# Performance work log

Hardware: AMD Instinct MI355X
Metric: run time of the kernel (lower is better)

## Reference

```python
import jax, jax.numpy as jnp
import numpy as np

N = 100000   # nodes
E = 1600000  # edges
NF = 128     # nfeat
NH = 64      # nhid
NC = 16      # nclass
C = 1.0      # curvature
EPS = 1e-15
PROJ_EPS = 4e-3  # float32 boundary eps used by HGCN PoincareBall
SQC = C ** 0.5


def _norm(v):
    return jnp.maximum(jnp.linalg.norm(v, axis=-1, keepdims=True), EPS)


def _artanh(v):
    return jnp.arctanh(jnp.clip(v, -1.0 + 1e-7, 1.0 - 1e-7))


def proj(p):
    # clip to the open ball of radius (1-eps)/sqrt(c)
    n = _norm(p)
    maxnorm = (1.0 - PROJ_EPS) / SQC
    return jnp.where(n > maxnorm, p / n * maxnorm, p)


def expmap0(u):
    n = _norm(u)
    return jnp.tanh(SQC * n) * u / (SQC * n)


def logmap0(p):
    n = _norm(p)
    return _artanh(SQC * n) * p / (SQC * n)


def mobius_add(x, y):
    x2 = jnp.sum(x * x, axis=-1, keepdims=True)
    y2 = jnp.sum(y * y, axis=-1, keepdims=True)
    xy = jnp.sum(x * y, axis=-1, keepdims=True)
    num = (1.0 + 2.0 * C * xy + C * y2) * x + (1.0 - C * x2) * y
    den = 1.0 + 2.0 * C * xy + (C ** 2) * x2 * y2
    return num / jnp.maximum(den, EPS)


def mobius_matvec(W, p):
    # W: [out, in], p: [N, in] on the ball
    pn = _norm(p)
    mp = p @ W.T  # [N, out]
    mpn = jnp.linalg.norm(mp, axis=-1, keepdims=True)
    res = jnp.tanh(mpn / pn * _artanh(SQC * pn)) * mp / (SQC * jnp.maximum(mpn, EPS))
    return jnp.where(mpn <= EPS, jnp.zeros_like(res), res)


def setup_inputs() -> dict:
    key = jax.random.key(0)
    ks = jax.random.split(key, 16)
    inp = {
        "x": jax.random.normal(ks[0], (N, NF), dtype=jnp.float32),
        "src": jax.random.randint(ks[1], (E,), 0, N, dtype=jnp.int32),
        "dst": jax.random.randint(ks[2], (E,), 0, N, dtype=jnp.int32),
        "adj_val": jax.random.uniform(ks[3], (E,), dtype=jnp.float32) * 0.0625,
        "W1": jax.random.normal(ks[4], (NH, NF), dtype=jnp.float32) / np.sqrt(NF),
        "b1": jnp.zeros((NH,), dtype=jnp.float32),
        "W2": jax.random.normal(ks[5], (NH, NH), dtype=jnp.float32) / np.sqrt(NH),
        "b2": jnp.zeros((NH,), dtype=jnp.float32),
        "W3": jax.random.normal(ks[6], (NH, NH), dtype=jnp.float32) / np.sqrt(NH),
        "b3": jnp.zeros((NH,), dtype=jnp.float32),
        "W4": jax.random.normal(ks[7], (NH // 2, NH), dtype=jnp.float32) / np.sqrt(NH),
        "b4": jnp.zeros((NH // 2,), dtype=jnp.float32),
        "W5": jax.random.normal(ks[8], (NC, NH // 2), dtype=jnp.float32) / np.sqrt(NH // 2),
        "b5": jnp.zeros((NC,), dtype=jnp.float32),
    }
    return inp


def _hgc_layer(h, W, b, src, dst, adj_val):
    # HypLinear: mobius matvec + hyperbolic bias
    res = proj(mobius_matvec(W, h))
    hyp_b = proj(expmap0(b[None, :]))
    res = proj(mobius_add(res, hyp_b))
    # HypAgg: aggregate in tangent space at origin via sparse adj
    ht = logmap0(res)                                   # [N, d]
    msg = adj_val[:, None] * ht[src]                    # [E, d]
    agg = jax.ops.segment_sum(msg, dst, num_segments=N)  # [N, d]
    res = proj(expmap0(agg))
    # HypAct: relu in tangent space, re-map to ball
    res = proj(expmap0(jax.nn.relu(logmap0(res))))
    return res


def reference(x, src, dst, adj_val, W1, b1, W2, b2, W3, b3, W4, b4, W5, b5):
    h = proj(expmap0(x))  # map Euclidean features to the ball (proj_tan0 = identity)
    h = _hgc_layer(h, W1, b1, src, dst, adj_val)
    h = _hgc_layer(h, W2, b2, src, dst, adj_val)
    h = _hgc_layer(h, W3, b3, src, dst, adj_val)
    t = logmap0(h)  # back to tangent space for the Euclidean head
    z = jax.nn.relu(t @ W4.T + b4)
    return jax.nn.log_softmax(z @ W5.T + b5, axis=-1)  # [N, nclass]
```

## Files before the change

### kernel.cpp

```cpp
#include <hip/hip_runtime.h>
#include <hip/hip_bf16.h>
#include <hip/hip_fp16.h>
#include <math.h>

#define NFEAT 128
#define NHID  64
#define ATH996 3.106303f
#define CHUNK 4096

typedef __attribute__((ext_vector_type(8))) short short8;
typedef __attribute__((ext_vector_type(4))) float floatx4;
typedef unsigned short ushort_t;
typedef unsigned long long u64;

__device__ __forceinline__ float wave_sum(float v) {
#pragma unroll
    for (int m = 1; m < 64; m <<= 1) v += __shfl_xor(v, m, 64);
    return v;
}

__device__ __forceinline__ float fast_tanh(float x) {
    float e = __expf(2.f * x);
    return 1.f - 2.f / (e + 1.f);
}

__device__ __forceinline__ float artanh_clip(float v) {
    const float lim = 0.99999988f;
    v = fminf(fmaxf(v, -lim), lim);
    return 0.5f * __logf((1.f + v) / (1.f - v));
}

__device__ __forceinline__ unsigned pack2(float a, float b) {
    __hip_bfloat16 x = __float2bfloat16(a), y = __float2bfloat16(b);
    ushort_t ux = *(ushort_t*)&x, uy = *(ushort_t*)&y;
    return (unsigned)ux | ((unsigned)uy << 16);
}

__device__ __forceinline__ ushort_t f2bf(float f) {
    __hip_bfloat16 h = __float2bfloat16(f);
    return *(ushort_t*)&h;
}

__device__ __forceinline__ float pe_adj(unsigned p) {
    return __half2float(__ushort_as_half((ushort_t)(p & 0x7fffu)));
}


__global__ __launch_bounds__(256) void k_bscan(const int* __restrict__ gBktCnt,
        int* __restrict__ gBktBase, int* __restrict__ gCur,
        int* __restrict__ off, int nb, int n, int e) {
    __shared__ int s[256];
    int tid = threadIdx.x;
    int base = tid * 4;
    int c0 = (base + 0 < nb) ? gBktCnt[base + 0] : 0;
    int c1 = (base + 1 < nb) ? gBktCnt[base + 1] : 0;
    int c2 = (base + 2 < nb) ? gBktCnt[base + 2] : 0;
    int c3 = (base + 3 < nb) ? gBktCnt[base + 3] : 0;
    int tsum = c0 + c1 + c2 + c3;
    s[tid] = tsum; __syncthreads();
    for (int o = 1; o < 256; o <<= 1) {
        int v = (tid >= o) ? s[tid - o] : 0;
        __syncthreads();
        s[tid] += v;
        __syncthreads();
    }
    int ex = s[tid] - tsum;
    int e0 = ex, e1 = ex + c0, e2 = ex + c0 + c1, e3 = ex + c0 + c1 + c2;
    if (base + 0 < nb) { gBktBase[base + 0] = e0; gCur[base + 0] = e0; }
    if (base + 1 < nb) { gBktBase[base + 1] = e1; gCur[base + 1] = e1; }
    if (base + 2 < nb) { gBktBase[base + 2] = e2; gCur[base + 2] = e2; }
    if (base + 3 < nb) { gBktBase[base + 3] = e3; gCur[base + 3] = e3; }
    if (tid == 255) gBktBase[nb] = s[255];
    if (tid == 0) off[n] = e;
}

__global__ __launch_bounds__(256) void k_bscatter(const int* __restrict__ dst,
        const int* __restrict__ src, const float* __restrict__ adj,
        int* __restrict__ gCur, u64* __restrict__ gStage, int e, int nb) {
    __shared__ u64 stage[CHUNK];
    __shared__ int cnt[512], excl[512], rcnt[512], myBase[512], s[256];
    int tid = threadIdx.x;
    int start = blockIdx.x * CHUNK, end = min(e, start + CHUNK);
    for (int t = tid; t < nb; t += 256) { cnt[t] = 0; rcnt[t] = 0; }
    __syncthreads();
    for (int i = start + tid; i < end; i += 256)
        atomicAdd(&cnt[dst[i] >> 8], 1);
    __syncthreads();
    int v0 = (2 * tid < nb) ? cnt[2 * tid] : 0;
    int v1 = (2 * tid + 1 < nb) ? cnt[2 * tid + 1] : 0;
    int tsum = v0 + v1;
    s[tid] = tsum; __syncthreads();
    for (int o = 1; o < 256; o <<= 1) {
        int v = (tid >= o) ? s[tid - o] : 0;
        __syncthreads();
        s[tid] += v;
        __syncthreads();
    }
    int ex = s[tid] - tsum;
    if (2 * tid < nb) excl[2 * tid] = ex;
    if (2 * tid + 1 < nb) excl[2 * tid + 1] = ex + v0;
    __syncthreads();
    for (int t = tid; t < nb; t += 256)
        if (cnt[t]) myBase[t] = atomicAdd(&gCur[t], cnt[t]);
    for (int i = start + tid; i < end; i += 256) {
        int d = dst[i];
        int b = d >> 8;
        unsigned ab = (unsigned)__half_as_ushort(__float2half(adj[i])) & 0x7fffu;
        u64 u = ((u64)(unsigned)d << 32) |
                (u64)(((unsigned)src[i] << 15) | ab);
        int r = atomicAdd(&rcnt[b], 1);
        stage[excl[b] + r] = u;
    }
    __syncthreads();
    int sz = end - start;
    for (int j = tid; j < sz; j += 256) {
        u64 u = stage[j];
        int b = (int)(u >> 40) & 0x1ff;
        gStage[myBase[b] + (j - excl[b])] = u;
    }
}

__global__ __launch_bounds__(256) void k_bfinal(const u64* __restrict__ gStage,
        const int* __restrict__ gBktBase, int* __restrict__ off,
        unsigned* __restrict__ pe, int n) {
    __shared__ int ncnt[256], nexcl[256], rcnt[256], s[256];
    int tid = threadIdx.x, b = blockIdx.x;
    int ebeg = gBktBase[b], eend = gBktBase[b + 1];
    int nbeg = b << 8;
    ncnt[tid] = 0; rcnt[tid] = 0;
    __syncthreads();
    for (int j = ebeg + tid; j < eend; j += 256) {
        int dl = ((int)(gStage[j] >> 32) & 0x1ffff) - nbeg;
        atomicAdd(&ncnt[dl], 1);
    }
    __syncthreads();
    int v = ncnt[tid];
    s[tid] = v; __syncthreads();
    for (int o = 1; o < 256; o <<= 1) {
        int t2 = (tid >= o) ? s[tid - o] : 0;
        __syncthreads();
        s[tid] += t2;
        __syncthreads();
    }
    nexcl[tid] = s[tid] - v;
    if (nbeg + tid < n) off[nbeg + tid] = ebeg + nexcl[tid];
    __syncthreads();
    for (int j = ebeg + tid; j < eend; j += 256) {
        u64 u = gStage[j];
        int dl = ((int)(u >> 32) & 0x1ffff) - nbeg;
        int r = atomicAdd(&rcnt[dl], 1);
        pe[ebeg + nexcl[dl] + r] = (unsigned)u;
    }
}

__global__ __launch_bounds__(256) void k_prep(
        const float* __restrict__ W1, const float* __restrict__ W2,
        const float* __restrict__ W3, const float* __restrict__ W4,
        const float* __restrict__ W5, const float* __restrict__ b1,
        const float* __restrict__ b2, const float* __restrict__ b3,
        ushort_t* __restrict__ Bpk1, ushort_t* __restrict__ Bpk2,
        ushort_t* __restrict__ Bpk3, ushort_t* __restrict__ Bpk4,
        ushort_t* __restrict__ Bpk5, float* __restrict__ hbs,
        float* __restrict__ hbns, int* __restrict__ gBktCnt, int nb) {
    int bid = blockIdx.x, tid = threadIdx.x;
    if (bid >= 75) {
        for (int t = tid; t < nb; t += 256) gBktCnt[t] = 0;
        return;
    }
    if (bid < 64) {
        const float* W; ushort_t* Bpk; int K, o;
        if (bid < 32)      { W = W1; Bpk = Bpk1; K = 128; o = bid * 256 + tid; }
        else if (bid < 48) { W = W2; Bpk = Bpk2; K = 64;  o = (bid - 32) * 256 + tid; }
        else               { W = W3; Bpk = Bpk3; K = 64;  o = (bid - 48) * 256 + tid; }
        int j = o & 7, c = (o >> 3) & 15, nf = (o >> 7) & 3, hi = (o >> 9) & 3,
            ks = o >> 11;
        Bpk[o] = f2bf(W[(nf * 16 + c) * K + ks * 32 + hi * 8 + j]);
    } else if (bid < 72) {
        int o = (bid - 64) * 256 + tid;
        int j = o & 7, c = (o >> 3) & 15, nf = (o >> 7) & 1, hi = (o >> 8) & 3,
            ks = o >> 10;
        Bpk4[o] = f2bf(W4[(nf * 16 + c) * 64 + ks * 32 + hi * 8 + j]);
    } else if (bid < 74) {
        int o = (bid - 72) * 256 + tid;
        if (o < 512) {
            int j = o & 7, c = (o >> 3) & 15, hi = o >> 7;
            Bpk5[o] = f2bf(W5[c * 32 + hi * 8 + j]);
        }
    } else {
        if (tid < 192) {
            int wv = tid >> 6, lane = tid & 63;
            const float* b = (wv == 0) ? b1 : (wv == 1) ? b2 : b3;
            float bv = b[lane];
            float bn = fmaxf(sqrtf(wave_sum(bv * bv)), 1e-15f);
            float th = fast_tanh(bn);
            float f = th / bn;
            float hn = th;
            if (th > 0.996f) { f = 0.996f / bn; hn = 0.996f; }
            hbs[wv * 64 + lane] = bv * f;
            if (lane == 0) hbns[wv] = hn;
        }
    }
}

__device__ __forceinline__ void epi_vals(const float vin[4], float pn,
        float hbn, const float* __restrict__ hb, int c, float outv[4]) {
    float pp = 0.f;
#pragma unroll
    for (int nf = 0; nf < 4; ++nf) pp += vin[nf] * vin[nf];
#pragma unroll
    for (int m = 1; m < 16; m <<= 1) pp += __shfl_xor(pp, m, 64);
    float mpn = sqrtf(pp);
    float an = artanh_clip(pn);
    if (hbn <= 1e-15f) {
        float targ = (mpn / pn) * an;
        float scale = (targ > ATH996) ? (ATH996 / mpn) : (an / pn);
        if (mpn <= 1e-15f) scale = 0.f;
#pragma unroll
        for (int nf = 0; nf < 4; ++nf) outv[nf] = vin[nf] * scale;
    } else {
        float targ = (mpn / pn) * an;
        float th = fast_tanh(targ);
        float rn = fminf(th, 0.996f);
        float rs = (mpn <= 1e-15f) ? 0.f : (rn / mpn);
        float res[4], xyp = 0.f;
#pragma unroll
        for (int nf = 0; nf < 4; ++nf) {
            res[nf] = vin[nf] * rs;
            xyp += res[nf] * hb[nf * 16 + c];
        }
#pragma unroll
        for (int m = 1; m < 16; m <<= 1) xyp += __shfl_xor(xyp, m, 64);
        float x2 = rn * rn, y2 = hbn * hbn;
        float den = fmaxf(1.f + 2.f * xyp + x2 * y2, 1e-15f);
        float ca = (1.f + 2.f * xyp + y2) / den, cb = (1.f - x2) / den;
        float mv[4], mm = 0.f;
#pragma unroll
        for (int nf = 0; nf < 4; ++nf) {
            mv[nf] = ca * res[nf] + cb * hb[nf * 16 + c];
            mm += mv[nf] * mv[nf];
        }
#pragma unroll
        for (int m = 1; m < 16; m <<= 1) mm += __shfl_xor(mm, m, 64);
        float mn = sqrtf(mm);
        float mc = fminf(fmaxf(mn, 1e-15f), 0.996f);
        float msc = ((mn > 0.996f) ? (0.996f / mn) : 1.f) * artanh_clip(mc) / mc;
#pragma unroll
        for (int nf = 0; nf < 4; ++nf) outv[nf] = mv[nf] * msc;
    }
}

__global__ __launch_bounds__(256) void k_gemm1_hist(
        const float* __restrict__ x, const ushort_t* __restrict__ Bpk,
        const float* __restrict__ hb, const float* __restrict__ hbn_p,
        ushort_t* __restrict__ htout, int n, int gBlocks,
        const int* __restrict__ dst, int* __restrict__ gBktCnt, int e, int nb) {
    constexpr int RB = 256;
    __shared__ __align__(16) unsigned char As[64 * RB];
    __shared__ float pns[64], fs[64];
    __shared__ int cnt[512];
    int tid = threadIdx.x;
    if ((int)blockIdx.x >= gBlocks) {
        for (int t = tid; t < nb; t += 256) cnt[t] = 0;
        __syncthreads();
        int start = ((int)blockIdx.x - gBlocks) * CHUNK, end = min(e, start + CHUNK);
        for (int i = start + tid; i < end; i += 256)
            atomicAdd(&cnt[dst[i] >> 8], 1);
        __syncthreads();
        for (int t = tid; t < nb; t += 256)
            if (cnt[t]) atomicAdd(&gBktCnt[t], cnt[t]);
        return;
    }
    int wv = tid >> 6, lane = tid & 63;
    int grp = lane >> 4, l = lane & 15;
    int rowBase = blockIdx.x * 64;
#pragma unroll
    for (int it = 0; it < 4; ++it) {
        int row = wv * 16 + it * 4 + grp, rg = rowBase + row;
        float4 va = make_float4(0.f, 0.f, 0.f, 0.f), vb = va;
        if (rg < n) {
            const float4* xr = (const float4*)(x + (size_t)rg * NFEAT + l * 8);
            va = xr[0]; vb = xr[1];
        }
        uint4 pk;
        pk.x = pack2(va.x, va.y); pk.y = pack2(va.z, va.w);
        pk.z = pack2(vb.x, vb.y); pk.w = pack2(vb.z, vb.w);
        unsigned byte = (unsigned)(row * RB + l * 16) ^ ((row & 7) << 4);
        *(uint4*)(As + byte) = pk;
        float ss = va.x * va.x + va.y * va.y + va.z * va.z + va.w * va.w +
                   vb.x * vb.x + vb.y * vb.y + vb.z * vb.z + vb.w * vb.w;
#pragma unroll
        for (int m = 1; m < 16; m <<= 1) ss += __shfl_xor(ss, m, 64);
        if (l == 0) {
            float nr = fmaxf(sqrtf(ss), 1e-15f);
            float th = fast_tanh(nr);
            float f = th / nr;
            float pn = fmaxf(th, 1e-15f);
            if (th > 0.996f) { f = 0.996f / nr; pn = 0.996f; }
            pns[row] = pn; fs[row] = f;
        }
    }
    int hi = lane >> 4, c = lane & 15;
    short8 bf[4][4];
#pragma unroll
    for (int ks = 0; ks < 4; ++ks)
#pragma unroll
        for (int nf = 0; nf < 4; ++nf)
            bf[ks][nf] = *(const short8*)(Bpk + (((size_t)(ks * 4 + hi) * 4 + nf) * 16 + c) * 8);
    floatx4 acc[4];
#pragma unroll
    for (int nf = 0; nf < 4; ++nf)
#pragma unroll
        for (int r = 0; r < 4; ++r) acc[nf][r] = 0.f;
    int arow = wv * 16 + c;
#pragma unroll
    for (int ks = 0; ks < 4; ++ks) {
        unsigned byte = (unsigned)(arow * RB + ks * 64 + hi * 16) ^ ((arow & 7) << 4);
        short8 af = *(const short8*)(As + byte);
#pragma unroll
        for (int nf = 0; nf < 4; ++nf)
            acc[nf] = __builtin_amdgcn_mfma_f32_16x16x32_bf16(af, bf[ks][nf], acc[nf], 0, 0, 0);
    }
    float hbn = hbn_p[0];
#pragma unroll
    for (int r = 0; r < 4; ++r) {
        int row = wv * 16 + hi * 4 + r, rg = rowBase + row;
        float f = fs[row];
        float vin[4], outv[4];
#pragma unroll
        for (int nf = 0; nf < 4; ++nf) vin[nf] = acc[nf][r] * f;
        epi_vals(vin, pns[row], hbn, hb, c, outv);
        if (rg < n) {
#pragma unroll
            for (int nf = 0; nf < 4; ++nf)
                htout[(size_t)rg * 64 + nf * 16 + c] = f2bf(outv[nf]);
        }
    }
}

__global__ __launch_bounds__(256) void k_gemm64(
        const ushort_t* __restrict__ h, const float* __restrict__ nrm_in,
        const ushort_t* __restrict__ Bpk, const float* __restrict__ hb,
        const float* __restrict__ hbn_p, ushort_t* __restrict__ htout, int n) {
    constexpr int RB = 128;
    __shared__ __align__(16) unsigned char As[64 * RB];
    int tid = threadIdx.x, wv = tid >> 6, lane = tid & 63;
    int grp = lane >> 4, l = lane & 15;
    int rowBase = blockIdx.x * 64;
#pragma unroll
    for (int it = 0; it < 4; ++it) {
        int row = wv * 16 + it * 4 + grp, rg = rowBase + row;
        uint2 pk = make_uint2(0u, 0u);
        if (rg < n) pk = *(const uint2*)(h + (size_t)rg * 64 + l * 4);
        unsigned byte = (unsigned)(row * RB + l * 8) ^ ((row & 7) << 4);
        *(uint2*)(As + byte) = pk;
    }
    int hi = lane >> 4, c = lane & 15;
    short8 bf[2][4];
#pragma unroll
    for (int ks = 0; ks < 2; ++ks)
#pragma unroll
        for (int nf = 0; nf < 4; ++nf)
            bf[ks][nf] = *(const short8*)(Bpk + (((size_t)(ks * 4 + hi) * 4 + nf) * 16 + c) * 8);
    floatx4 acc[4];
#pragma unroll
    for (int nf = 0; nf < 4; ++nf)
#pragma unroll
        for (int r = 0; r < 4; ++r) acc[nf][r] = 0.f;
    int arow = wv * 16 + c;
#pragma unroll
    for (int ks = 0; ks < 2; ++ks) {
        unsigned byte = (unsigned)(arow * RB + ks * 64 + hi * 16) ^ ((arow & 7) << 4);
        short8 af = *(const short8*)(As + byte);
#pragma unroll
        for (int nf = 0; nf < 4; ++nf)
            acc[nf] = __builtin_amdgcn_mfma_f32_16x16x32_bf16(af, bf[ks][nf], acc[nf], 0, 0, 0);
    }
    float hbn = hbn_p[0];
#pragma unroll
    for (int r = 0; r < 4; ++r) {
        int row = wv * 16 + hi * 4 + r, rg = rowBase + row;
        float pn = (rg < n) ? nrm_in[rg] : 1e-15f;
        float vin[4], outv[4];
#pragma unroll
        for (int nf = 0; nf < 4; ++nf) vin[nf] = acc[nf][r];
        epi_vals(vin, pn, hbn, hb, c, outv);
        if (rg < n) {
#pragma unroll
            for (int nf = 0; nf < 4; ++nf)
                htout[(size_t)rg * 64 + nf * 16 + c] = f2bf(outv[nf]);
        }
    }
}

template <bool TANGENT_OUT>
__global__ __launch_bounds__(256) void k_agg_act(
        const ushort_t* __restrict__ ht, const int* __restrict__ off,
        const unsigned* __restrict__ pe, ushort_t* __restrict__ hout,
        float* __restrict__ nrm_out, int n) {
    int tid = threadIdx.x;
    int grp = tid >> 4, l = tid & 15;
    int gw = (tid & 63) >> 4;
    int node = blockIdx.x * 16 + grp;
    if (node >= n) return;
    int beg = off[node], end = off[node + 1];
    const char* hb8 = (const char*)ht + l * 8;
    float ac[4][4] = {};
    for (int e = beg; e < end; e += 16) {
        int cnt = end - e;
        unsigned pv = (l < cnt) ? pe[e + l] : 0u;
        uint2 rr[16];
#pragma unroll
        for (int u = 0; u < 16; ++u) {
            unsigned p = __shfl(pv, (gw << 4) | u, 64);
            unsigned row = (u < cnt) ? (p >> 15) : 0u;
            rr[u] = *(const uint2*)(hb8 + ((size_t)row << 7));
        }
#pragma unroll
        for (int u = 0; u < 16; ++u) {
            unsigned p = __shfl(pv, (gw << 4) | u, 64);
            float w = (u < cnt) ? pe_adj(p) : 0.f;
            ac[u & 3][0] = fmaf(w, __uint_as_float(rr[u].x << 16), ac[u & 3][0]);
            ac[u & 3][1] = fmaf(w, __uint_as_float(rr[u].x & 0xffff0000u), ac[u & 3][1]);
            ac[u & 3][2] = fmaf(w, __uint_as_float(rr[u].y << 16), ac[u & 3][2]);
            ac[u & 3][3] = fmaf(w, __uint_as_float(rr[u].y & 0xffff0000u), ac[u & 3][3]);
        }
    }
    float f0 = (ac[0][0] + ac[1][0]) + (ac[2][0] + ac[3][0]);
    float f1 = (ac[0][1] + ac[1][1]) + (ac[2][1] + ac[3][1]);
    float f2 = (ac[0][2] + ac[1][2]) + (ac[2][2] + ac[3][2]);
    float f3 = (ac[0][3] + ac[1][3]) + (ac[2][3] + ac[3][3]);
    float ss = f0 * f0 + f1 * f1 + f2 * f2 + f3 * f3;
#pragma unroll
    for (int m = 1; m < 16; m <<= 1) ss += __shfl_xor(ss, m, 64);
    float un = fmaxf(sqrtf(ss), 1e-15f);
    float thu = fast_tanh(un);
    float pf = thu / un, pn = thu;
    if (thu > 0.996f) { pf = 0.996f / un; pn = 0.996f; }
    float pnc = fmaxf(pn, 1e-15f);
    float ls = artanh_clip(pnc) / pnc * pf;
    float t0 = fmaxf(ls * f0, 0.f), t1 = fmaxf(ls * f1, 0.f);
    float t2 = fmaxf(ls * f2, 0.f), t3 = fmaxf(ls * f3, 0.f);
    float ss2 = t0 * t0 + t1 * t1 + t2 * t2 + t3 * t3;
#pragma unroll
    for (int m = 1; m < 16; m <<= 1) ss2 += __shfl_xor(ss2, m, 64);
    float tn = fmaxf(sqrtf(ss2), 1e-15f);
    uint2 ov;
    if (TANGENT_OUT) {
        float sc = (tn > ATH996) ? (ATH996 / tn) : 1.f;
        ov = make_uint2(pack2(t0 * sc, t1 * sc), pack2(t2 * sc, t3 * sc));
    } else {
        float tht = fast_tanh(tn);
        float rf = tht / tn, rn = tht;
        if (tht > 0.996f) { rf = 0.996f / tn; rn = 0.996f; }
        ov = make_uint2(pack2(rf * t0, rf * t1), pack2(rf * t2, rf * t3));
        if (l == 0) nrm_out[node] = fmaxf(rn, 1e-15f);
    }
    *(uint2*)((char*)hout + (size_t)node * 128 + l * 8) = ov;
}

__global__ __launch_bounds__(256) void k_head(
        const ushort_t* __restrict__ t_in, const ushort_t* __restrict__ Bpk4,
        const float* __restrict__ b4, const ushort_t* __restrict__ Bpk5,
        const float* __restrict__ b5, float* __restrict__ out, int n) {
    constexpr int RB = 128;
    __shared__ __align__(16) unsigned char As[64 * RB];
    __shared__ __align__(16) unsigned char Zs[4][16 * 80];
    int tid = threadIdx.x, wv = tid >> 6, lane = tid & 63;
    int grp = lane >> 4, l = lane & 15;
    int rowBase = blockIdx.x * 64;
#pragma unroll
    for (int it = 0; it < 4; ++it) {
        int row = wv * 16 + it * 4 + grp, rg = rowBase + row;
        uint2 pk = make_uint2(0u, 0u);
        if (rg < n) pk = *(const uint2*)(t_in + (size_t)rg * 64 + l * 4);
        unsigned byte = (unsigned)(row * RB + l * 8) ^ ((row & 7) << 4);
        *(uint2*)(As + byte) = pk;
    }
    int hi = lane >> 4, c = lane & 15;
    short8 bf4[2][2];
#pragma unroll
    for (int ks = 0; ks < 2; ++ks)
#pragma unroll
        for (int nf = 0; nf < 2; ++nf)
            bf4[ks][nf] = *(const short8*)(Bpk4 + (((size_t)(ks * 4 + hi) * 2 + nf) * 16 + c) * 8);
    floatx4 acc[2];
#pragma unroll
    for (int nf = 0; nf < 2; ++nf)
#pragma unroll
        for (int r = 0; r < 4; ++r) acc[nf][r] = 0.f;
    int arow = wv * 16 + c;
#pragma unroll
    for (int ks = 0; ks < 2; ++ks) {
        unsigned byte = (unsigned)(arow * RB + ks * 64 + hi * 16) ^ ((arow & 7) << 4);
        short8 af = *(const short8*)(As + byte);
#pragma unroll
        for (int nf = 0; nf < 2; ++nf)
            acc[nf] = __builtin_amdgcn_mfma_f32_16x16x32_bf16(af, bf4[ks][nf], acc[nf], 0, 0, 0);
    }
    float bb0 = b4[c], bb1 = b4[16 + c];
#pragma unroll
    for (int r = 0; r < 4; ++r) {
        int zr = hi * 4 + r;
        *(ushort_t*)(Zs[wv] + zr * 80 + c * 2) = f2bf(fmaxf(acc[0][r] + bb0, 0.f));
        *(ushort_t*)(Zs[wv] + zr * 80 + (16 + c) * 2) = f2bf(fmaxf(acc[1][r] + bb1, 0.f));
    }
    short8 bf5 = *(const short8*)(Bpk5 + ((size_t)(hi * 16 + c)) * 8);
    short8 zf = *(const short8*)(Zs[wv] + c * 80 + hi * 16);
    floatx4 acc5;
#pragma unroll
    for (int r = 0; r < 4; ++r) acc5[r] = 0.f;
    acc5 = __builtin_amdgcn_mfma_f32_16x16x32_bf16(zf, bf5, acc5, 0, 0, 0);
    float b5v = b5[c];
#pragma unroll
    for (int r = 0; r < 4; ++r) {
        float y = acc5[r] + b5v;
        float mx = y;
#pragma unroll
        for (int mk = 1; mk < 16; mk <<= 1) mx = fmaxf(mx, __shfl_xor(mx, mk, 64));
        float sm = __expf(y - mx);
#pragma unroll
        for (int mk = 1; mk < 16; mk <<= 1) sm += __shfl_xor(sm, mk, 64);
        int rg = rowBase + wv * 16 + hi * 4 + r;
        if (rg < n) out[(size_t)rg * 16 + c] = y - mx - __logf(sm);
    }
}

extern "C" void kernel_launch(void* const* d_in, const int* in_sizes, int n_in,
                              void* d_out, int out_size, void* d_ws, size_t ws_size,
                              hipStream_t stream) {
    const float* x   = (const float*)d_in[0];
    const int*   src = (const int*)d_in[1];
    const int*   dst = (const int*)d_in[2];
    const float* adj = (const float*)d_in[3];
    const float* W1  = (const float*)d_in[4];  const float* b1 = (const float*)d_in[5];
    const float* W2  = (const float*)d_in[6];  const float* b2 = (const float*)d_in[7];
    const float* W3  = (const float*)d_in[8];  const float* b3 = (const float*)d_in[9];
    const float* W4  = (const float*)d_in[10]; const float* b4 = (const float*)d_in[11];
    const float* W5  = (const float*)d_in[12]; const float* b5 = (const float*)d_in[13];
    float* out = (float*)d_out;

    const int N = in_sizes[0] / NFEAT;
    const int E = in_sizes[1];
    const int NB = (N + 255) >> 8;

    char* w = (char*)d_ws;
    auto alloc = [&](size_t bytes) {
        char* p = w; w += (bytes + 255) & ~(size_t)255; return p;
    };
    int* off      = (int*)alloc((size_t)(N + 1) * 4);
    int* gBktCnt  = (int*)alloc((size_t)NB * 4);
    int* gBktBase = (int*)alloc((size_t)(NB + 1) * 4);
    int* gCur     = (int*)alloc((size_t)NB * 4);
    u64* gStage   = (u64*)alloc((size_t)E * 8);
    unsigned* pe  = (unsigned*)alloc((size_t)E * 4);
    ushort_t* B   = (ushort_t*)alloc((size_t)N * 64 * 2);
    ushort_t* D   = (ushort_t*)alloc((size_t)N * 64 * 2);
    float* nrm    = (float*)alloc((size_t)N * 4);
    float* hbs    = (float*)alloc(192 * 4);
    float* hbns   = (float*)alloc(4 * 4);
    ushort_t* Bpk1 = (ushort_t*)alloc(8192 * 2);
    ushort_t* Bpk2 = (ushort_t*)alloc(4096 * 2);
    ushort_t* Bpk3 = (ushort_t*)alloc(4096 * 2);
    ushort_t* Bpk4 = (ushort_t*)alloc(2048 * 2);
    ushort_t* Bpk5 = (ushort_t*)alloc(512 * 2);

    dim3 blk(256);
    int aggBlocks  = (N + 15) / 16;
    int gemmBlocks = (N + 63) / 64;
    int sortBlocks = (E + CHUNK - 1) / CHUNK;

    k_prep<<<76, blk, 0, stream>>>(W1, W2, W3, W4, W5, b1, b2, b3,
                                   Bpk1, Bpk2, Bpk3, Bpk4, Bpk5, hbs, hbns,
                                   gBktCnt, NB);

    k_gemm1_hist<<<gemmBlocks + sortBlocks, blk, 0, stream>>>(
        x, Bpk1, hbs, hbns, B, N, gemmBlocks, dst, gBktCnt, E, NB);

    k_bscan<<<1, blk, 0, stream>>>(gBktCnt, gBktBase, gCur, off, NB, N, E);
    k_bscatter<<<sortBlocks, blk, 0, stream>>>(dst, src, adj, gCur, gStage, E, NB);
    k_bfinal<<<NB, blk, 0, stream>>>(gStage, gBktBase, off, pe, N);

    k_agg_act<false><<<aggBlocks, blk, 0, stream>>>(B, off, pe, D, nrm, N);
    k_gemm64<<<gemmBlocks, blk, 0, stream>>>(D, nrm, Bpk2, hbs + 64, hbns + 1, B, N);
    k_agg_act<false><<<aggBlocks, blk, 0, stream>>>(B, off, pe, D, nrm, N);
    k_gemm64<<<gemmBlocks, blk, 0, stream>>>(D, nrm, Bpk3, hbs + 128, hbns + 2, B, N);
    k_agg_act<true><<<aggBlocks, blk, 0, stream>>>(B, off, pe, D, nullptr, N);

    k_head<<<gemmBlocks, blk, 0, stream>>>(D, Bpk4, b4, Bpk5, b5, out, N);
}
```

Before: 222.5 us.

## Switch intermediate storage and MFMA to fp16 with packed half2 aggregation

```diff
diff --git a/kernel.cpp b/kernel.cpp
--- a/kernel.cpp
+++ b/kernel.cpp
@@ -1,5 +1,4 @@
 #include <hip/hip_runtime.h>
-#include <hip/hip_bf16.h>
 #include <hip/hip_fp16.h>
 #include <math.h>
 
@@ -8,7 +7,7 @@
 #define ATH996 3.106303f
 #define CHUNK 4096
 
-typedef __attribute__((ext_vector_type(8))) short short8;
+typedef __attribute__((ext_vector_type(8))) _Float16 half8;
 typedef __attribute__((ext_vector_type(4))) float floatx4;
 typedef unsigned short ushort_t;
 typedef unsigned long long u64;
@@ -30,19 +29,17 @@
     return 0.5f * __logf((1.f + v) / (1.f - v));
 }
 
-__device__ __forceinline__ unsigned pack2(float a, float b) {
-    __hip_bfloat16 x = __float2bfloat16(a), y = __float2bfloat16(b);
-    ushort_t ux = *(ushort_t*)&x, uy = *(ushort_t*)&y;
-    return (unsigned)ux | ((unsigned)uy << 16);
-}
-
-__device__ __forceinline__ ushort_t f2bf(float f) {
-    __hip_bfloat16 h = __float2bfloat16(f);
+__device__ __forceinline__ ushort_t f2h(float f) {
+    __half h = __float2half(f);
     return *(ushort_t*)&h;
 }
 
-__device__ __forceinline__ float pe_adj(unsigned p) {
-    return __half2float(__ushort_as_half((ushort_t)(p & 0x7fffu)));
+__device__ __forceinline__ unsigned pk2h(float a, float b) {
+    return (unsigned)f2h(a) | ((unsigned)f2h(b) << 16);
+}
+
+__device__ __forceinline__ __half pe_adjh(unsigned p) {
+    return __ushort_as_half((ushort_t)(p & 0x7fffu));
 }
 
 
@@ -174,17 +171,17 @@
         else               { W = W3; Bpk = Bpk3; K = 64;  o = (bid - 48) * 256 + tid; }
         int j = o & 7, c = (o >> 3) & 15, nf = (o >> 7) & 3, hi = (o >> 9) & 3,
             ks = o >> 11;
-        Bpk[o] = f2bf(W[(nf * 16 + c) * K + ks * 32 + hi * 8 + j]);
+        Bpk[o] = f2h(W[(nf * 16 + c) * K + ks * 32 + hi * 8 + j]);
     } else if (bid < 72) {
         int o = (bid - 64) * 256 + tid;
         int j = o & 7, c = (o >> 3) & 15, nf = (o >> 7) & 1, hi = (o >> 8) & 3,
             ks = o >> 10;
-        Bpk4[o] = f2bf(W4[(nf * 16 + c) * 64 + ks * 32 + hi * 8 + j]);
+        Bpk4[o] = f2h(W4[(nf * 16 + c) * 64 + ks * 32 + hi * 8 + j]);
     } else if (bid < 74) {
         int o = (bid - 72) * 256 + tid;
         if (o < 512) {
             int j = o & 7, c = (o >> 3) & 15, hi = o >> 7;
-            Bpk5[o] = f2bf(W5[c * 32 + hi * 8 + j]);
+            Bpk5[o] = f2h(W5[c * 32 + hi * 8 + j]);
         }
     } else {
         if (tid < 192) {
@@ -282,8 +279,8 @@
             va = xr[0]; vb = xr[1];
         }
         uint4 pk;
-        pk.x = pack2(va.x, va.y); pk.y = pack2(va.z, va.w);
-        pk.z = pack2(vb.x, vb.y); pk.w = pack2(vb.z, vb.w);
+        pk.x = pk2h(va.x, va.y); pk.y = pk2h(va.z, va.w);
+        pk.z = pk2h(vb.x, vb.y); pk.w = pk2h(vb.z, vb.w);
         unsigned byte = (unsigned)(row * RB + l * 16) ^ ((row & 7) << 4);
         *(uint4*)(As + byte) = pk;
         float ss = va.x * va.x + va.y * va.y + va.z * va.z + va.w * va.w +
@@ -300,12 +297,12 @@
         }
     }
     int hi = lane >> 4, c = lane & 15;
-    short8 bf[4][4];
+    half8 bf[4][4];
 #pragma unroll
     for (int ks = 0; ks < 4; ++ks)
 #pragma unroll
         for (int nf = 0; nf < 4; ++nf)
-            bf[ks][nf] = *(const short8*)(Bpk + (((size_t)(ks * 4 + hi) * 4 + nf) * 16 + c) * 8);
+            bf[ks][nf] = *(const half8*)(Bpk + (((size_t)(ks * 4 + hi) * 4 + nf) * 16 + c) * 8);
     floatx4 acc[4];
 #pragma unroll
     for (int nf = 0; nf < 4; ++nf)
@@ -315,10 +312,10 @@
 #pragma unroll
     for (int ks = 0; ks < 4; ++ks) {
         unsigned byte = (unsigned)(arow * RB + ks * 64 + hi * 16) ^ ((arow & 7) << 4);
-        short8 af = *(const short8*)(As + byte);
+        half8 af = *(const half8*)(As + byte);
 #pragma unroll
         for (int nf = 0; nf < 4; ++nf)
-            acc[nf] = __builtin_amdgcn_mfma_f32_16x16x32_bf16(af, bf[ks][nf], acc[nf], 0, 0, 0);
+            acc[nf] = __builtin_amdgcn_mfma_f32_16x16x32_f16(af, bf[ks][nf], acc[nf], 0, 0, 0);
     }
     float hbn = hbn_p[0];
 #pragma unroll
@@ -332,7 +329,7 @@
         if (rg < n) {
 #pragma unroll
             for (int nf = 0; nf < 4; ++nf)
-                htout[(size_t)rg * 64 + nf * 16 + c] = f2bf(outv[nf]);
+                htout[(size_t)rg * 64 + nf * 16 + c] = f2h(outv[nf]);
         }
     }
 }
@@ -355,12 +352,12 @@
         *(uint2*)(As + byte) = pk;
     }
     int hi = lane >> 4, c = lane & 15;
-    short8 bf[2][4];
+    half8 bf[2][4];
 #pragma unroll
     for (int ks = 0; ks < 2; ++ks)
 #pragma unroll
         for (int nf = 0; nf < 4; ++nf)
-            bf[ks][nf] = *(const short8*)(Bpk + (((size_t)(ks * 4 + hi) * 4 + nf) * 16 + c) * 8);
+            bf[ks][nf] = *(const half8*)(Bpk + (((size_t)(ks * 4 + hi) * 4 + nf) * 16 + c) * 8);
     floatx4 acc[4];
 #pragma unroll
     for (int nf = 0; nf < 4; ++nf)
@@ -370,10 +367,10 @@
 #pragma unroll
     for (int ks = 0; ks < 2; ++ks) {
         unsigned byte = (unsigned)(arow * RB + ks * 64 + hi * 16) ^ ((arow & 7) << 4);
-        short8 af = *(const short8*)(As + byte);
+        half8 af = *(const half8*)(As + byte);
 #pragma unroll
         for (int nf = 0; nf < 4; ++nf)
-            acc[nf] = __builtin_amdgcn_mfma_f32_16x16x32_bf16(af, bf[ks][nf], acc[nf], 0, 0, 0);
+            acc[nf] = __builtin_amdgcn_mfma_f32_16x16x32_f16(af, bf[ks][nf], acc[nf], 0, 0, 0);
     }
     float hbn = hbn_p[0];
 #pragma unroll
@@ -387,7 +384,7 @@
         if (rg < n) {
 #pragma unroll
             for (int nf = 0; nf < 4; ++nf)
-                htout[(size_t)rg * 64 + nf * 16 + c] = f2bf(outv[nf]);
+                htout[(size_t)rg * 64 + nf * 16 + c] = f2h(outv[nf]);
         }
     }
 }
@@ -399,36 +396,46 @@
         float* __restrict__ nrm_out, int n) {
     int tid = threadIdx.x;
     int grp = tid >> 4, l = tid & 15;
-    int gw = (tid & 63) >> 4;
     int node = blockIdx.x * 16 + grp;
     if (node >= n) return;
     int beg = off[node], end = off[node + 1];
     const char* hb8 = (const char*)ht + l * 8;
-    float ac[4][4] = {};
-    for (int e = beg; e < end; e += 16) {
-        int cnt = end - e;
-        unsigned pv = (l < cnt) ? pe[e + l] : 0u;
-        uint2 rr[16];
-#pragma unroll
-        for (int u = 0; u < 16; ++u) {
-            unsigned p = __shfl(pv, (gw << 4) | u, 64);
-            unsigned row = (u < cnt) ? (p >> 15) : 0u;
-            rr[u] = *(const uint2*)(hb8 + ((size_t)row << 7));
-        }
-#pragma unroll
-        for (int u = 0; u < 16; ++u) {
-            unsigned p = __shfl(pv, (gw << 4) | u, 64);
-            float w = (u < cnt) ? pe_adj(p) : 0.f;
-            ac[u & 3][0] = fmaf(w, __uint_as_float(rr[u].x << 16), ac[u & 3][0]);
-            ac[u & 3][1] = fmaf(w, __uint_as_float(rr[u].x & 0xffff0000u), ac[u & 3][1]);
-            ac[u & 3][2] = fmaf(w, __uint_as_float(rr[u].y << 16), ac[u & 3][2]);
-            ac[u & 3][3] = fmaf(w, __uint_as_float(rr[u].y & 0xffff0000u), ac[u & 3][3]);
-        }
-    }
-    float f0 = (ac[0][0] + ac[1][0]) + (ac[2][0] + ac[3][0]);
-    float f1 = (ac[0][1] + ac[1][1]) + (ac[2][1] + ac[3][1]);
-    float f2 = (ac[0][2] + ac[1][2]) + (ac[2][2] + ac[3][2]);
-    float f3 = (ac[0][3] + ac[1][3]) + (ac[2][3] + ac[3][3]);
+    __half2 ax[4], ay[4];
+#pragma unroll
+    for (int u = 0; u < 4; ++u) {
+        ax[u] = __float2half2_rn(0.f);
+        ay[u] = __float2half2_rn(0.f);
+    }
+    int e = beg;
+    for (; e + 7 < end; e += 8) {
+        unsigned p[8];
+#pragma unroll
+        for (int u = 0; u < 8; ++u) p[u] = pe[e + u];
+        uint2 rr[8];
+#pragma unroll
+        for (int u = 0; u < 8; ++u)
+            rr[u] = *(const uint2*)(hb8 + ((size_t)(p[u] >> 15) << 7));
+#pragma unroll
+        for (int u = 0; u < 8; ++u) {
+            __half2 w2 = __half2half2(pe_adjh(p[u]));
+            ax[u & 3] = __hfma2(w2, *(__half2*)&rr[u].x, ax[u & 3]);
+            ay[u & 3] = __hfma2(w2, *(__half2*)&rr[u].y, ay[u & 3]);
+        }
+    }
+    for (; e < end; ++e) {
+        unsigned p = pe[e];
+        uint2 r = *(const uint2*)(hb8 + ((size_t)(p >> 15) << 7));
+        __half2 w2 = __half2half2(pe_adjh(p));
+        ax[0] = __hfma2(w2, *(__half2*)&r.x, ax[0]);
+        ay[0] = __hfma2(w2, *(__half2*)&r.y, ay[0]);
+    }
+    float f0 = 0.f, f1 = 0.f, f2 = 0.f, f3 = 0.f;
+#pragma unroll
+    for (int u = 0; u < 4; ++u) {
+        float2 vx = __half22float2(ax[u]);
+        float2 vy = __half22float2(ay[u]);
+        f0 += vx.x; f1 += vx.y; f2 += vy.x; f3 += vy.y;
+    }
     float ss = f0 * f0 + f1 * f1 + f2 * f2 + f3 * f3;
 #pragma unroll
     for (int m = 1; m < 16; m <<= 1) ss += __shfl_xor(ss, m, 64);
@@ -447,12 +454,12 @@
     uint2 ov;
     if (TANGENT_OUT) {
         float sc = (tn > ATH996) ? (ATH996 / tn) : 1.f;
-        ov = make_uint2(pack2(t0 * sc, t1 * sc), pack2(t2 * sc, t3 * sc));
+        ov = make_uint2(pk2h(t0 * sc, t1 * sc), pk2h(t2 * sc, t3 * sc));
     } else {
         float tht = fast_tanh(tn);
         float rf = tht / tn, rn = tht;
         if (tht > 0.996f) { rf = 0.996f / tn; rn = 0.996f; }
-        ov = make_uint2(pack2(rf * t0, rf * t1), pack2(rf * t2, rf * t3));
+        ov = make_uint2(pk2h(rf * t0, rf * t1), pk2h(rf * t2, rf * t3));
         if (l == 0) nrm_out[node] = fmaxf(rn, 1e-15f);
     }
     *(uint2*)((char*)hout + (size_t)node * 128 + l * 8) = ov;
@@ -477,12 +484,12 @@
         *(uint2*)(As + byte) = pk;
     }
     int hi = lane >> 4, c = lane & 15;
-    short8 bf4[2][2];
+    half8 bf4[2][2];
 #pragma unroll
     for (int ks = 0; ks < 2; ++ks)
 #pragma unroll
         for (int nf = 0; nf < 2; ++nf)
-            bf4[ks][nf] = *(const short8*)(Bpk4 + (((size_t)(ks * 4 + hi) * 2 + nf) * 16 + c) * 8);
+            bf4[ks][nf] = *(const half8*)(Bpk4 + (((size_t)(ks * 4 + hi) * 2 + nf) * 16 + c) * 8);
     floatx4 acc[2];
 #pragma unroll
     for (int nf = 0; nf < 2; ++nf)
@@ -492,24 +499,24 @@
 #pragma unroll
     for (int ks = 0; ks < 2; ++ks) {
         unsigned byte = (unsigned)(arow * RB + ks * 64 + hi * 16) ^ ((arow & 7) << 4);
-        short8 af = *(const short8*)(As + byte);
+        half8 af = *(const half8*)(As + byte);
 #pragma unroll
         for (int nf = 0; nf < 2; ++nf)
-            acc[nf] = __builtin_amdgcn_mfma_f32_16x16x32_bf16(af, bf4[ks][nf], acc[nf], 0, 0, 0);
+            acc[nf] = __builtin_amdgcn_mfma_f32_16x16x32_f16(af, bf4[ks][nf], acc[nf], 0, 0, 0);
     }
     float bb0 = b4[c], bb1 = b4[16 + c];
 #pragma unroll
     for (int r = 0; r < 4; ++r) {
         int zr = hi * 4 + r;
-        *(ushort_t*)(Zs[wv] + zr * 80 + c * 2) = f2bf(fmaxf(acc[0][r] + bb0, 0.f));
-        *(ushort_t*)(Zs[wv] + zr * 80 + (16 + c) * 2) = f2bf(fmaxf(acc[1][r] + bb1, 0.f));
-    }
-    short8 bf5 = *(const short8*)(Bpk5 + ((size_t)(hi * 16 + c)) * 8);
-    short8 zf = *(const short8*)(Zs[wv] + c * 80 + hi * 16);
+        *(ushort_t*)(Zs[wv] + zr * 80 + c * 2) = f2h(fmaxf(acc[0][r] + bb0, 0.f));
+        *(ushort_t*)(Zs[wv] + zr * 80 + (16 + c) * 2) = f2h(fmaxf(acc[1][r] + bb1, 0.f));
+    }
+    half8 bf5 = *(const half8*)(Bpk5 + ((size_t)(hi * 16 + c)) * 8);
+    half8 zf = *(const half8*)(Zs[wv] + c * 80 + hi * 16);
     floatx4 acc5;
 #pragma unroll
     for (int r = 0; r < 4; ++r) acc5[r] = 0.f;
-    acc5 = __builtin_amdgcn_mfma_f32_16x16x32_bf16(zf, bf5, acc5, 0, 0, 0);
+    acc5 = __builtin_amdgcn_mfma_f32_16x16x32_f16(zf, bf5, acc5, 0, 0, 0);
     float b5v = b5[c];
 #pragma unroll
     for (int r = 0; r < 4; ++r) {
```

Result: no change. 222.9 us (+0.2%).
